# Kernel tuning notes

Measured on AMD Instinct MI355X. Metric: run time of the kernel, lower is better.

## Reference

```python
import jax, jax.numpy as jnp
import numpy as np

V0, V1 = 0.1, 0.2  # SSD encode/decode variances
LEVEL_WS = [160, 80, 40, 20, 10, 5]
BOUNDS = [0, 25600, 32000, 33600, 34000, 34100, 34125]
A_TOTAL = 34125
CLS_W, LOC_W = 1.0, 2.0

def _to_cxcywh(a):
    return np.stack([(a[:, 0] + a[:, 2]) / 2.0, (a[:, 1] + a[:, 3]) / 2.0,
                     a[:, 2] - a[:, 0], a[:, 3] - a[:, 1]], 1)

def _decode(d, anc):
    xy = anc[:, :2] + d[:, :2] * V0 * anc[:, 2:]
    wh = anc[:, 2:] * np.exp(d[:, 2:] * V1)
    return np.concatenate([xy - wh / 2.0, xy + wh / 2.0], 1)

def _encode(anc, gt):
    gcx = (gt[:, 0] + gt[:, 2]) / 2.0; gcy = (gt[:, 1] + gt[:, 3]) / 2.0
    gw = gt[:, 2] - gt[:, 0]; gh = gt[:, 3] - gt[:, 1]
    return np.stack([(gcx - anc[:, 0]) / (anc[:, 2] * V0),
                     (gcy - anc[:, 1]) / (anc[:, 3] * V0),
                     np.log(np.maximum(gw, 1e-6) / anc[:, 2]) / V1,
                     np.log(np.maximum(gh, 1e-6) / anc[:, 3]) / V1], 1)

def _relabel(conf, bbox_targets, anchors):
    # Faithful mirror of the torch.no_grad() relabel loop: per-image per-level
    # decode, unique-with-counts, center-distance top-k, sigmoid-score sort,
    # scatter relabel. Data-dependent shapes, so done in numpy (no grads flow here).
    conf = np.asarray(conf); bt = np.array(bbox_targets, copy=True); anc = np.asarray(anchors)
    tanc = _to_cxcywh(anc)
    labels = bt[:, :, -1].copy()
    for b in range(conf.shape[0]):
        pos = bt[b, :, -1] == 1
        uniq = []
        for li in range(6):
            s, e = BOUNDS[li], BOUNDS[li + 1]
            m = pos[s:e]
            dec = _decode(bt[b, s:e][m][:, :4], tanc[s:e][m])
            uniq.append(np.unique(np.round(dec, 3), axis=0, return_counts=True))
        start_idx, end_idx, tmp_w = -25600, 0, 160.0
        for li, (u, c) in enumerate(uniq):
            if li > 4:
                continue
            if u.shape[0] == 0:
                continue
            max_num = int(c.max())
            start_idx += int(tmp_w ** 2); end_idx += int(tmp_w ** 2); tmp_w /= 2.0
            s, e = start_idx, end_idx
            ctr = tanc[s:e, :2]
            for ti in range(u.shape[0]):
                n_match = int(c[ti])
                if n_match == max_num:
                    continue
                gt = u[ti]
                dist = np.hypot(ctr[:, 0] - (gt[0] + gt[2]) / 2.0, ctr[:, 1] - (gt[1] + gt[3]) / 2.0)
                cand = np.argsort(dist, kind='stable')[:max_num]
                scores = 1.0 / (1.0 + np.exp(-conf[b, s + cand, 0]))
                order = np.argsort(scores, kind='stable')
                rel = cand[order[-(max_num - n_match):]] + s
                rel = rel[labels[b, rel] != 1]
                if rel.shape[0] == 0:
                    continue
                bt[b, rel, :4] = _encode(tanc[rel], np.repeat(gt[None, :], rel.shape[0], 0))
                bt[b, rel, 4] = 1.0
                labels[b, rel] = 1.0
    return labels.astype(np.float32), bt.astype(np.float32)

def _losses(conf, loc, labels, bt):
    # cls: sigmoid BCE-with-logits summed, normalized by num positives
    # loc: smooth-L1 on encoded deltas over positive anchors, same normalization
    tgt = (labels == 1).astype(conf.dtype)
    z = conf[..., 0]
    bce = jnp.maximum(z, 0) - z * tgt + jnp.log1p(jnp.exp(-jnp.abs(z)))
    num_pos = jnp.maximum(tgt.sum(), 1.0)
    cls_loss = CLS_W * bce.sum() / num_pos
    d = loc - bt[..., :4]
    sl1 = jnp.where(jnp.abs(d) < 1.0, 0.5 * d * d, jnp.abs(d) - 0.5)
    loc_loss = LOC_W * (sl1 * tgt[..., None]).sum() / num_pos
    return cls_loss, loc_loss, cls_loss + loc_loss

def setup_inputs() -> dict:
    rng = np.random.RandomState(0)
    B, NGT = 16, 8
    anchors = []
    for w in LEVEL_WS:
        stride = 640.0 / w
        t = (np.arange(w) + 0.5) * stride
        cy, cx = np.meshgrid(t, t, indexing='ij')
        cx = cx.reshape(-1); cy = cy.reshape(-1); sz = 4.0 * stride
        anchors.append(np.stack([cx - sz / 2, cy - sz / 2, cx + sz / 2, cy + sz / 2], 1))
    anchors = np.concatenate(anchors, 0).astype(np.float32)  # [34125, 4]
    tanc = _to_cxcywh(anchors)
    bt = np.zeros((B, A_TOTAL, 5), np.float32)
    bt[:, :, :4] = rng.randn(B, A_TOTAL, 4).astype(np.float32) * 0.1
    gts = np.zeros((B, NGT, 4), np.float32)
    for b in range(B):
        for g in range(NGT):
            cx, cy = rng.uniform(64, 576, 2); sz = rng.uniform(16, 256)
            gt = np.array([cx - sz / 2, cy - sz / 2, cx + sz / 2, cy + sz / 2], np.float32)
            gts[b, g] = gt
            li = int(rng.randint(0, 5))
            s, e = BOUNDS[li], BOUNDS[li + 1]
            k = int(rng.randint(2, 20))
            idx = rng.choice(e - s, size=k, replace=False) + s
            bt[b, idx, :4] = _encode(tanc[idx], np.repeat(gt[None, :], k, 0)).astype(np.float32)
            bt[b, idx, 4] = 1.0
    conf = rng.randn(B, A_TOTAL, 1).astype(np.float32)
    loc = (rng.randn(B, A_TOTAL, 4) * 0.1).astype(np.float32)
    return {"conf": jnp.asarray(conf), "loc": jnp.asarray(loc),
            "bbox_targets": jnp.asarray(bt), "anchors": jnp.asarray(anchors),
            "bbox_labels_list": jnp.asarray(gts)}

def reference(conf, loc, bbox_targets, anchors, bbox_labels_list):
    labels, bt = _relabel(conf, bbox_targets, anchors)
    return _losses(conf, loc, jnp.asarray(labels), jnp.asarray(bt))
```

## Files before the change

kernel.cpp:

```cpp
#include <hip/hip_runtime.h>
#include <cstdint>
#include <cstddef>

#define A_TOTAL 34125
#define BATCH 16
#define NBA (BATCH * A_TOTAL)
#define SBT 1024
#define PT2 25
#define NB 1024
#define CAND 768
#define NSEG (BATCH * 5)
#define CCAP 16384
#define SELGRID 160
#define SCAN_GRID 1024
#define SCAN_THR 256

__device__ __constant__ int d_bounds[7] = {0, 25600, 32000, 33600, 34000, 34100, 34125};

#define MAXU 48
#define MAXPOS 512
#define MAXC 32
#define CLAIM_NONE 0x7FFFFFFF

__global__ __launch_bounds__(SCAN_THR)
void scan_kernel(const float* __restrict__ bt,
                 const float* __restrict__ anchors,
                 const float* __restrict__ conf,
                 const float* __restrict__ loc,
                 int* __restrict__ claim,
                 uint8_t* __restrict__ posmap,
                 float* __restrict__ part,
                 int* __restrict__ ccnt,
                 float2* __restrict__ ctr) {
    const int tid = threadIdx.x;
    const int gtid = blockIdx.x * blockDim.x + tid;
    const int gsz = gridDim.x * blockDim.x;
    if (gtid == 0) *ccnt = 0;

    int4* c4 = (int4*)claim;
    for (int i = gtid; i < NBA / 4; i += gsz)
        c4[i] = make_int4(CLAIM_NONE, CLAIM_NONE, CLAIM_NONE, CLAIM_NONE);
    for (int a = gtid; a < A_TOTAL; a += gsz) {
        const float4 ar = reinterpret_cast<const float4*>(anchors)[a];
        ctr[a] = make_float2((ar.x + ar.z) / 2.0f, (ar.y + ar.w) / 2.0f);
    }

    float bce = 0.0f, pos = 0.0f, l1 = 0.0f;

    const float4* cf4 = (const float4*)conf;
    for (int i = gtid; i < NBA / 4; i += gsz) {
        const float4 z4 = cf4[i];
        const float zz[4] = {z4.x, z4.y, z4.z, z4.w};
        #pragma unroll
        for (int c = 0; c < 4; ++c) {
            const float z = zz[c];
            bce += fmaxf(z, 0.0f) + log1pf(expf(-fabsf(z)));
        }
    }

    const float4* btv = (const float4*)bt;
    const int nchunk = NBA * 5 / 4;
    for (int f4 = gtid; f4 < nchunk; f4 += gsz) {
        const float4 v = btv[f4];
        const unsigned g0 = (unsigned)f4 * 4u;
        const unsigned m = g0 % 5u;
        if (m != 0u) {
            const unsigned c = 4u - m;
            const float val = (c == 0u) ? v.x : (c == 1u) ? v.y : (c == 2u) ? v.z : v.w;
            const unsigned i = (g0 + c) / 5u;
            const bool p = (val == 1.0f);
            posmap[i] = p ? 1 : 0;
            if (p) {
                bce -= conf[i];
                pos += 1.0f;
                const float* tp = bt + (size_t)i * 5u;
                const float4 lv4 = reinterpret_cast<const float4*>(loc)[i];
                const float dv[4] = {lv4.x - tp[0], lv4.y - tp[1],
                                     lv4.z - tp[2], lv4.w - tp[3]};
                #pragma unroll
                for (int cc = 0; cc < 4; ++cc) {
                    const float ad = fabsf(dv[cc]);
                    l1 += (ad < 1.0f) ? 0.5f * dv[cc] * dv[cc] : ad - 0.5f;
                }
            }
        }
    }

    for (int off = 32; off > 0; off >>= 1) {
        bce += __shfl_down(bce, off);
        pos += __shfl_down(pos, off);
        l1  += __shfl_down(l1, off);
    }
    __shared__ float sb[3][4];
    const int wid = tid >> 6, lane = tid & 63;
    if (lane == 0) { sb[0][wid] = bce; sb[1][wid] = pos; sb[2][wid] = l1; }
    __syncthreads();
    if (tid == 0) {
        float B = 0, P = 0, L = 0;
        #pragma unroll
        for (int w = 0; w < 4; ++w) { B += sb[0][w]; P += sb[1][w]; L += sb[2][w]; }
        part[blockIdx.x * 3 + 0] = B;
        part[blockIdx.x * 3 + 1] = P;
        part[blockIdx.x * 3 + 2] = L;
    }
}

__global__ __launch_bounds__(256)
void dedup_kernel(const float* __restrict__ bt,
                  const float* __restrict__ anchors,
                  const uint8_t* __restrict__ posmap,
                  float* __restrict__ uq,
                  int* __restrict__ uc,
                  int* __restrict__ nu_out,
                  int* __restrict__ mn_out,
                  int* __restrict__ wl,
                  int* __restrict__ wlc)
{
    const int b = blockIdx.x / 5;
    const int lv = blockIdx.x % 5;
    const int seg = blockIdx.x;
    const unsigned bA = (unsigned)b * A_TOTAL;
    const int tid = threadIdx.x;

    __shared__ int s_pos[MAXPOS];
    __shared__ float t0[MAXPOS], t1[MAXPOS], t2[MAXPOS], t3[MAXPOS];
    __shared__ int s_cnt[MAXPOS];
    __shared__ uint8_t s_rep[MAXPOS];
    __shared__ int s_ucs[MAXU];
    __shared__ int s_np, s_nu;

    if (tid == 0) { s_np = 0; s_nu = 0; }
    __syncthreads();

    {
        const unsigned gs = bA + (unsigned)d_bounds[lv];
        const unsigned ge = bA + (unsigned)d_bounds[lv + 1];
        const unsigned astart = (gs + 15u) & ~15u;
        const unsigned aend_raw = ge & ~15u;
        const unsigned hend = min(astart, ge);
        for (unsigned g = gs + tid; g < hend; g += blockDim.x)
            if (posmap[g]) {
                int p = atomicAdd(&s_np, 1);
                if (p < MAXPOS) s_pos[p] = (int)(g - bA);
            }
        if (aend_raw > astart) {
            const uint4* pm4 = (const uint4*)(posmap + astart);
            const unsigned n16 = (aend_raw - astart) >> 4;
            for (unsigned c = tid; c < n16; c += blockDim.x) {
                const uint4 v = pm4[c];
                if (v.x | v.y | v.z | v.w) {
                    const unsigned base = astart + (c << 4);
                    const unsigned wv[4] = {v.x, v.y, v.z, v.w};
                    #pragma unroll
                    for (int w = 0; w < 4; ++w) {
                        #pragma unroll
                        for (int byi = 0; byi < 4; ++byi) {
                            if ((wv[w] >> (8 * byi)) & 0xffu) {
                                int p = atomicAdd(&s_np, 1);
                                if (p < MAXPOS)
                                    s_pos[p] = (int)(base + 4u * w + byi - bA);
                            }
                        }
                    }
                }
            }
            for (unsigned g = aend_raw + tid; g < ge; g += blockDim.x)
                if (posmap[g]) {
                    int p = atomicAdd(&s_np, 1);
                    if (p < MAXPOS) s_pos[p] = (int)(g - bA);
                }
        }
    }
    __syncthreads();
    const int np_ = min(s_np, MAXPOS);

    for (int p = tid; p < np_; p += blockDim.x) {
        int a = s_pos[p];
        const float* ar = anchors + (size_t)a * 4;
        float acx = (ar[0] + ar[2]) / 2.0f;
        float acy = (ar[1] + ar[3]) / 2.0f;
        float aw = ar[2] - ar[0];
        float ah = ar[3] - ar[1];
        const float* dd = bt + ((size_t)bA + a) * 5;
        float cx = acx + (dd[0] * 0.1f) * aw;
        float cy = acy + (dd[1] * 0.1f) * ah;
        float w = aw * expf(dd[2] * 0.2f);
        float h = ah * expf(dd[3] * 0.2f);
        t0[p] = rintf((cx - w / 2.0f) * 1000.0f) / 1000.0f;
        t1[p] = rintf((cy - h / 2.0f) * 1000.0f) / 1000.0f;
        t2[p] = rintf((cx + w / 2.0f) * 1000.0f) / 1000.0f;
        t3[p] = rintf((cy + h / 2.0f) * 1000.0f) / 1000.0f;
    }
    __syncthreads();

    for (int p = tid; p < np_; p += blockDim.x) {
        const float p0 = t0[p], p1 = t1[p], p2 = t2[p], p3 = t3[p];
        int cnt = 0, firstq = np_;
        for (int q = 0; q < np_; ++q) {
            bool eq = (t0[q] == p0) && (t1[q] == p1) && (t2[q] == p2) && (t3[q] == p3);
            if (eq) { cnt++; if (q < firstq) firstq = q; }
        }
        s_cnt[p] = cnt;
        bool rep = (firstq == p);
        s_rep[p] = rep ? 1 : 0;
        if (rep) atomicAdd(&s_nu, 1);
    }
    __syncthreads();

    float* uqp = uq + (size_t)seg * MAXU * 4;
    int* ucp = uc + (size_t)seg * MAXU;
    for (int p = tid; p < np_; p += blockDim.x) {
        if (!s_rep[p]) continue;
        const float p0 = t0[p], p1 = t1[p], p2 = t2[p], p3 = t3[p];
        int rank = 0;
        for (int q = 0; q < np_; ++q) {
            if (!s_rep[q]) continue;
            float q0 = t0[q], q1 = t1[q], q2 = t2[q], q3 = t3[q];
            bool lt = (q0 < p0) || (q0 == p0 && (q1 < p1 ||
                      (q1 == p1 && (q2 < p2 || (q2 == p2 && q3 < p3)))));
            if (lt) rank++;
        }
        if (rank < MAXU) {
            uqp[rank * 4 + 0] = p0; uqp[rank * 4 + 1] = p1;
            uqp[rank * 4 + 2] = p2; uqp[rank * 4 + 3] = p3;
            ucp[rank] = s_cnt[p];
            s_ucs[rank] = s_cnt[p];
        }
    }
    __syncthreads();

    if (tid == 0) {
        const int nu = min(s_nu, MAXU);
        nu_out[seg] = nu;
        int mn = 0;
        for (int j = 0; j < nu; ++j) mn = max(mn, s_ucs[j]);
        mn_out[seg] = mn;
        int n = 0;
        for (int ti = 0; ti < nu; ++ti)
            if (s_ucs[ti] != mn) wl[seg * MAXU + n++] = seg * MAXU + ti;
        wlc[seg] = n;
    }
}

__global__ __launch_bounds__(SBT)
void select_kernel(const float* __restrict__ conf,
                   const float2* __restrict__ ctr,
                   const float* __restrict__ uq,
                   const int* __restrict__ uc,
                   const int* __restrict__ nu_,
                   const int* __restrict__ mn_,
                   const int* __restrict__ wl,
                   const int* __restrict__ wlc,
                   int* __restrict__ claim,
                   int2* __restrict__ clist,
                   int* __restrict__ ccnt) {
    const int tid = threadIdx.x;

    __shared__ int s_hist[NB];
    __shared__ unsigned long long s_cand[CAND];
    __shared__ unsigned long long s_srt[MAXC];
    __shared__ float s_sc[MAXC];
    __shared__ int s_c, s_B;

    for (int w = blockIdx.x; ; w += gridDim.x) {
        int cum = 0, ent = -1;
        for (int i = 0; i < NSEG; ++i) {
            int c = wlc[i];
            if (ent < 0 && w < cum + c) ent = wl[i * MAXU + (w - cum)];
            cum += c;
        }
        if (w >= cum) return;

        const int ti = ent % MAXU;
        const int sg = ent / MAXU;
        const int li = sg % 5;
        const int b  = sg / 5;

        int nus[5];
        #pragma unroll
        for (int l = 0; l < 5; ++l) nus[l] = nu_[b * 5 + l];

        int s = -25600;
        float tmpw = 160.0f;
        for (int l = 0; l <= li; ++l) {
            if (nus[l] != 0) { s += (int)(tmpw * tmpw); tmpw *= 0.5f; }
        }

        const int mn = mn_[sg];
        const int cnt = uc[(size_t)sg * MAXU + ti];
        const int need = mn - cnt;
        const int K = min(mn, MAXC);
        const unsigned bA = (unsigned)b * A_TOTAL;

        const float* g = uq + ((size_t)sg * MAXU + ti) * 4;
        const float gcx = (g[0] + g[2]) / 2.0f;
        const float gcy = (g[1] + g[3]) / 2.0f;

        float cxr[PT2], cyr[PT2];
        #pragma unroll
        for (int i = 0; i < PT2; ++i) {
            const float2 c = ctr[s + tid + (i << 10)];
            cxr[i] = c.x;
            cyr[i] = c.y;
        }

        s_hist[tid] = 0;
        if (tid == 0) s_c = 0;
        __syncthreads();

        #pragma unroll
        for (int i = 0; i < PT2; ++i) {
            float d = hypotf(cxr[i] - gcx, cyr[i] - gcy);
            int bin = min(NB - 1, (int)d);
            atomicAdd(&s_hist[bin], 1);
        }
        __syncthreads();

        if (tid < 64) {
            const int base = tid << 4;
            int part[16], psum = 0;
            #pragma unroll
            for (int i = 0; i < 16; ++i) { part[i] = s_hist[base + i]; psum += part[i]; }
            int run = psum;
            #pragma unroll
            for (int off = 1; off < 64; off <<= 1) {
                int o = __shfl_up(run, off);
                if (tid >= off) run += o;
            }
            const int excl = run - psum;
            if (excl < K && excl + psum >= K) {
                int c = excl, bs = base + 15;
                for (int i = 0; i < 16; ++i) { c += part[i]; if (c >= K) { bs = base + i; break; } }
                s_B = bs;
            }
        }
        __syncthreads();
        const int B = s_B;

        #pragma unroll
        for (int i = 0; i < PT2; ++i) {
            float d = hypotf(cxr[i] - gcx, cyr[i] - gcy);
            int bin = min(NB - 1, (int)d);
            if (bin <= B) {
                int p = atomicAdd(&s_c, 1);
                if (p < CAND)
                    s_cand[p] = (((unsigned long long)__float_as_uint(d)) << 32) |
                                (unsigned)(tid + (i << 10));
            }
        }
        __syncthreads();
        const int C = min(s_c, CAND);

        if (tid < C) {
            const unsigned long long mykey = s_cand[tid];
            int rank = 0;
            for (int j = 0; j < C; ++j) rank += (s_cand[j] < mykey) ? 1 : 0;
            if (rank < K) s_srt[rank] = mykey;
        }
        __syncthreads();

        if (tid < K) {
            const int o = (int)(s_srt[tid] & 0xffffffffULL);
            const float z = conf[bA + s + o];
            s_sc[tid] = 1.0f / (1.0f + expf(-z));
        }
        __syncthreads();

        if (tid < K) {
            const float my = s_sc[tid];
            int r = 0;
            for (int j = 0; j < K; ++j) {
                const float oj = s_sc[j];
                r += (oj > my || (oj == my && j > tid)) ? 1 : 0;
            }
            if (r < need) {
                const int o = (int)(s_srt[tid] & 0xffffffffULL);
                const int idx = (int)(bA + s + o);
                const int seq = li * MAXU + ti;
                atomicMin(&claim[idx], seq);
                int p = atomicAdd(ccnt, 1);
                if (p < CCAP) clist[p] = make_int2(idx, seq);
            }
        }
        __syncthreads();
    }
}

__global__ __launch_bounds__(1024)
void finalize_kernel(const float* __restrict__ conf,
                     const float* __restrict__ loc,
                     const float* __restrict__ bt,
                     const float* __restrict__ anchors,
                     const float* __restrict__ uq,
                     const int2* __restrict__ clist,
                     const int* __restrict__ ccnt,
                     const int* __restrict__ claim,
                     const float* __restrict__ part,
                     float* __restrict__ out) {
    const int tid = threadIdx.x;
    float bce = 0.0f, pos = 0.0f, l1 = 0.0f;
    const int cn = min(*ccnt, CCAP);
    for (int e = tid; e < cn; e += blockDim.x) {
        const int2 ent = clist[e];
        const int idx = ent.x;
        if (claim[idx] != ent.y) continue;
        if (bt[(size_t)idx * 5 + 4] == 1.0f) continue;
        bce -= conf[idx];
        pos += 1.0f;
        const int uli = ent.y / MAXU;
        const int uti = ent.y - uli * MAXU;
        const int b = idx / A_TOTAL;
        const int a = idx - b * A_TOTAL;
        const float* g = uq + ((size_t)(b * 5 + uli) * MAXU + uti) * 4;
        const float g0 = g[0], g1 = g[1], g2 = g[2], g3 = g[3];
        const float gcx = (g0 + g2) / 2.0f, gcy = (g1 + g3) / 2.0f;
        const float gw = g2 - g0, gh = g3 - g1;
        const float* ar = anchors + (size_t)a * 4;
        const float acx = (ar[0] + ar[2]) / 2.0f;
        const float acy = (ar[1] + ar[3]) / 2.0f;
        const float aw = ar[2] - ar[0];
        const float ah = ar[3] - ar[1];
        float ep[4];
        ep[0] = (gcx - acx) / (aw * 0.1f);
        ep[1] = (gcy - acy) / (ah * 0.1f);
        ep[2] = logf(fmaxf(gw, 1e-6f) / aw) / 0.2f;
        ep[3] = logf(fmaxf(gh, 1e-6f) / ah) / 0.2f;
        const float4 lvv = reinterpret_cast<const float4*>(loc)[idx];
        const float lvf[4] = {lvv.x, lvv.y, lvv.z, lvv.w};
        #pragma unroll
        for (int c = 0; c < 4; ++c) {
            const float dd = lvf[c] - ep[c];
            const float ad = fabsf(dd);
            l1 += (ad < 1.0f) ? 0.5f * dd * dd : ad - 0.5f;
        }
    }

    if (tid < SCAN_GRID) {
        bce += part[tid * 3 + 0];
        pos += part[tid * 3 + 1];
        l1  += part[tid * 3 + 2];
    }

    for (int off = 32; off > 0; off >>= 1) {
        bce += __shfl_down(bce, off);
        pos += __shfl_down(pos, off);
        l1  += __shfl_down(l1, off);
    }
    __shared__ float sb[3][16];
    const int wid = tid >> 6, lane = tid & 63;
    if (lane == 0) { sb[0][wid] = bce; sb[1][wid] = pos; sb[2][wid] = l1; }
    __syncthreads();
    if (tid == 0) {
        float B = 0, P = 0, L = 0;
        #pragma unroll
        for (int w = 0; w < 16; ++w) { B += sb[0][w]; P += sb[1][w]; L += sb[2][w]; }
        const double a0 = (double)B;
        const double a1 = (double)P;
        const double a2 = (double)L;
        const double np_ = a1 > 1.0 ? a1 : 1.0;
        const double cls = a0 / np_;
        const double lcl = 2.0 * a2 / np_;
        out[0] = (float)cls;
        out[1] = (float)lcl;
        out[2] = (float)(cls + lcl);
    }
}

extern "C" void kernel_launch(void* const* d_in, const int* in_sizes, int n_in,
                              void* d_out, int out_size, void* d_ws, size_t ws_size,
                              hipStream_t stream) {
    const float* conf    = (const float*)d_in[0];
    const float* loc     = (const float*)d_in[1];
    const float* bt      = (const float*)d_in[2];
    const float* anchors = (const float*)d_in[3];
    float* out = (float*)d_out;

    char* ws = (char*)d_ws;
    size_t off = 0;
    int* ccnt       = (int*)(ws + off);    off += 64;
    float* part     = (float*)(ws + off);  off += (size_t)SCAN_GRID * 3 * sizeof(float);
    int* claim      = (int*)(ws + off);    off += (size_t)NBA * sizeof(int);
    uint8_t* posmap = (uint8_t*)(ws + off); off += ((size_t)NBA + 63) & ~63ull;
    float* uq       = (float*)(ws + off);  off += (size_t)NSEG * MAXU * 4 * sizeof(float);
    int* uc         = (int*)(ws + off);    off += (size_t)NSEG * MAXU * sizeof(int);
    int* nu_        = (int*)(ws + off);    off += (size_t)NSEG * sizeof(int);
    int* mn_        = (int*)(ws + off);    off += (size_t)NSEG * sizeof(int);
    int* wl         = (int*)(ws + off);    off += (size_t)NSEG * MAXU * sizeof(int);
    int* wlc        = (int*)(ws + off);    off += ((size_t)NSEG * sizeof(int) + 15) & ~15ull;
    int2* clist     = (int2*)(ws + off);   off += (size_t)CCAP * sizeof(int2);
    float2* ctr     = (float2*)(ws + off); off += (size_t)A_TOTAL * sizeof(float2);

    scan_kernel<<<SCAN_GRID, SCAN_THR, 0, stream>>>(bt, anchors, conf, loc, claim,
                                                    posmap, part, ccnt, ctr);
    dedup_kernel<<<NSEG, 256, 0, stream>>>(bt, anchors, posmap, uq, uc, nu_, mn_,
                                           wl, wlc);
    select_kernel<<<SELGRID, SBT, 0, stream>>>(conf, ctr, uq, uc, nu_, mn_, wl, wlc,
                                               claim, clist, ccnt);
    finalize_kernel<<<1, 1024, 0, stream>>>(conf, loc, bt, anchors, uq, clist, ccnt,
                                            claim, part, out);
}
```

Measured before the change: 56.30 us.

## Fold finalize into select kernel via last-block-done reduction

```diff
diff --git a/kernel.cpp b/kernel.cpp
--- a/kernel.cpp
+++ b/kernel.cpp
@@ -31,11 +31,12 @@
                  uint8_t* __restrict__ posmap,
                  float* __restrict__ part,
                  int* __restrict__ ccnt,
+                 int* __restrict__ done_cnt,
                  float2* __restrict__ ctr) {
     const int tid = threadIdx.x;
     const int gtid = blockIdx.x * blockDim.x + tid;
     const int gsz = gridDim.x * blockDim.x;
-    if (gtid == 0) *ccnt = 0;
+    if (gtid == 0) { *ccnt = 0; *done_cnt = 0; }
 
     int4* c4 = (int4*)claim;
     for (int i = gtid; i < NBA / 4; i += gsz)
@@ -244,6 +245,9 @@
 
 __global__ __launch_bounds__(SBT)
 void select_kernel(const float* __restrict__ conf,
+                   const float* __restrict__ loc,
+                   const float* __restrict__ bt,
+                   const float* __restrict__ anchors,
                    const float2* __restrict__ ctr,
                    const float* __restrict__ uq,
                    const int* __restrict__ uc,
@@ -252,15 +256,18 @@
                    const int* __restrict__ wl,
                    const int* __restrict__ wlc,
                    int* __restrict__ claim,
-                   int2* __restrict__ clist,
-                   int* __restrict__ ccnt) {
+                   unsigned* __restrict__ clist,
+                   int* __restrict__ ccnt,
+                   int* __restrict__ done_cnt,
+                   const float* __restrict__ part,
+                   float* __restrict__ out) {
     const int tid = threadIdx.x;
 
     __shared__ int s_hist[NB];
     __shared__ unsigned long long s_cand[CAND];
     __shared__ unsigned long long s_srt[MAXC];
     __shared__ float s_sc[MAXC];
-    __shared__ int s_c, s_B;
+    __shared__ int s_c, s_B, s_last;
 
     for (int w = blockIdx.x; ; w += gridDim.x) {
         int cum = 0, ent = -1;
@@ -269,7 +276,7 @@
             if (ent < 0 && w < cum + c) ent = wl[i * MAXU + (w - cum)];
             cum += c;
         }
-        if (w >= cum) return;
+        if (w >= cum) break;
 
         const int ti = ent % MAXU;
         const int sg = ent / MAXU;
@@ -318,9 +325,9 @@
 
         if (tid < 64) {
             const int base = tid << 4;
-            int part[16], psum = 0;
+            int prt[16], psum = 0;
             #pragma unroll
-            for (int i = 0; i < 16; ++i) { part[i] = s_hist[base + i]; psum += part[i]; }
+            for (int i = 0; i < 16; ++i) { prt[i] = s_hist[base + i]; psum += prt[i]; }
             int run = psum;
             #pragma unroll
             for (int off = 1; off < 64; off <<= 1) {
@@ -330,7 +337,7 @@
             const int excl = run - psum;
             if (excl < K && excl + psum >= K) {
                 int c = excl, bs = base + 15;
-                for (int i = 0; i < 16; ++i) { c += part[i]; if (c >= K) { bs = base + i; break; } }
+                for (int i = 0; i < 16; ++i) { c += prt[i]; if (c >= K) { bs = base + i; break; } }
                 s_B = bs;
             }
         }
@@ -379,36 +386,33 @@
                 const int seq = li * MAXU + ti;
                 atomicMin(&claim[idx], seq);
                 int p = atomicAdd(ccnt, 1);
-                if (p < CCAP) clist[p] = make_int2(idx, seq);
-            }
-        }
-        __syncthreads();
-    }
-}
-
-__global__ __launch_bounds__(1024)
-void finalize_kernel(const float* __restrict__ conf,
-                     const float* __restrict__ loc,
-                     const float* __restrict__ bt,
-                     const float* __restrict__ anchors,
-                     const float* __restrict__ uq,
-                     const int2* __restrict__ clist,
-                     const int* __restrict__ ccnt,
-                     const int* __restrict__ claim,
-                     const float* __restrict__ part,
-                     float* __restrict__ out) {
-    const int tid = threadIdx.x;
+                if (p < CCAP)
+                    atomicExch(&clist[p], ((unsigned)idx << 8) | (unsigned)seq);
+            }
+        }
+        __syncthreads();
+    }
+
+    __syncthreads();
+    if (tid == 0) {
+        __threadfence();
+        s_last = (atomicAdd(done_cnt, 1) == gridDim.x - 1) ? 1 : 0;
+    }
+    __syncthreads();
+    if (!s_last) return;
+
     float bce = 0.0f, pos = 0.0f, l1 = 0.0f;
-    const int cn = min(*ccnt, CCAP);
+    const int cn = min(atomicAdd(ccnt, 0), CCAP);
     for (int e = tid; e < cn; e += blockDim.x) {
-        const int2 ent = clist[e];
-        const int idx = ent.x;
-        if (claim[idx] != ent.y) continue;
+        const unsigned pack = atomicAdd(&clist[e], 0u);
+        const int idx = (int)(pack >> 8);
+        const int seq = (int)(pack & 0xffu);
+        if (atomicAdd(&claim[idx], 0) != seq) continue;
         if (bt[(size_t)idx * 5 + 4] == 1.0f) continue;
         bce -= conf[idx];
         pos += 1.0f;
-        const int uli = ent.y / MAXU;
-        const int uti = ent.y - uli * MAXU;
+        const int uli = seq / MAXU;
+        const int uti = seq - uli * MAXU;
         const int b = idx / A_TOTAL;
         const int a = idx - b * A_TOTAL;
         const float* g = uq + ((size_t)(b * 5 + uli) * MAXU + uti) * 4;
@@ -477,7 +481,8 @@
 
     char* ws = (char*)d_ws;
     size_t off = 0;
-    int* ccnt       = (int*)(ws + off);    off += 64;
+    int* ccnt       = (int*)(ws + off);
+    int* done_cnt   = (int*)(ws + 32);     off += 64;
     float* part     = (float*)(ws + off);  off += (size_t)SCAN_GRID * 3 * sizeof(float);
     int* claim      = (int*)(ws + off);    off += (size_t)NBA * sizeof(int);
     uint8_t* posmap = (uint8_t*)(ws + off); off += ((size_t)NBA + 63) & ~63ull;
@@ -487,15 +492,14 @@
     int* mn_        = (int*)(ws + off);    off += (size_t)NSEG * sizeof(int);
     int* wl         = (int*)(ws + off);    off += (size_t)NSEG * MAXU * sizeof(int);
     int* wlc        = (int*)(ws + off);    off += ((size_t)NSEG * sizeof(int) + 15) & ~15ull;
-    int2* clist     = (int2*)(ws + off);   off += (size_t)CCAP * sizeof(int2);
+    unsigned* clist = (unsigned*)(ws + off); off += (size_t)CCAP * sizeof(unsigned);
     float2* ctr     = (float2*)(ws + off); off += (size_t)A_TOTAL * sizeof(float2);
 
     scan_kernel<<<SCAN_GRID, SCAN_THR, 0, stream>>>(bt, anchors, conf, loc, claim,
-                                                    posmap, part, ccnt, ctr);
+                                                    posmap, part, ccnt, done_cnt, ctr);
     dedup_kernel<<<NSEG, 256, 0, stream>>>(bt, anchors, posmap, uq, uc, nu_, mn_,
                                            wl, wlc);
-    select_kernel<<<SELGRID, SBT, 0, stream>>>(conf, ctr, uq, uc, nu_, mn_, wl, wlc,
-                                               claim, clist, ccnt);
-    finalize_kernel<<<1, 1024, 0, stream>>>(conf, loc, bt, anchors, uq, clist, ccnt,
-                                            claim, part, out);
+    select_kernel<<<SELGRID, SBT, 0, stream>>>(conf, loc, bt, anchors, ctr, uq, uc,
+                                               nu_, mn_, wl, wlc, claim, clist, ccnt,
+                                               done_cnt, part, out);
 }
```

New measurement: 57.15 us. No clear change (+1.5%).
